# Kernel tuning notes

Hardware: AMD Instinct MI355X
Metric: run time of the kernel (lower is better)

## Reference

```python
import jax, jax.numpy as jnp
import numpy as np

B, N, R = 16, 512, 10
DE, DR, DOUT = 256, 64, 256

def setup_inputs() -> dict:
    key = jax.random.key(0)
    k1, k2, k3, k4 = jax.random.split(key, 4)
    node_features = jax.random.normal(k1, (B, N, DE), dtype=jnp.float32)
    relation_features = jax.random.normal(k2, (B, R, DR), dtype=jnp.float32)
    adj = jax.random.uniform(k3, (B, R, N, N), dtype=jnp.float32)
    in_dim = (DE + DR) * R
    bound = float(np.sqrt(6.0 / (in_dim + DOUT)))  # xavier_uniform
    W = jax.random.uniform(k4, (DOUT, in_dim), dtype=jnp.float32, minval=-bound, maxval=bound)
    bias = jnp.zeros((DOUT,), dtype=jnp.float32)
    return {"node_features": node_features, "relation_features": relation_features,
            "adj": adj, "W": W, "bias": bias}

def reference(node_features, relation_features, adj, W, bias):
    # adj: [B,R,N,N]; node_features: [B,N,De]; relation_features: [B,R,Dr]
    # Per relation r: bmm(adj[:,r], cat([node, rel_r broadcast], -1))
    # Node part: adj @ node_features for every relation at once.
    node_part = jnp.einsum('brnm,bmd->brnd', adj, node_features)      # [B,R,N,De]
    # Relation part: adj @ (rel_r repeated over rows) == rowsum(adj) * rel_r
    rel_part = adj.sum(axis=-1)[..., None] * relation_features[:, :, None, :]  # [B,R,N,Dr]
    supports = jnp.concatenate([node_part, rel_part], axis=-1)        # [B,R,N,De+Dr]
    supports = supports.transpose(0, 2, 1, 3).reshape(node_features.shape[0],
                                                      node_features.shape[1], -1)  # [B,N,R*(De+Dr)]
    return supports @ W.T + bias
```

## Files before the change

kernel.cpp:

```cpp
#include <hip/hip_runtime.h>
#include <stdint.h>

#define B_     16
#define N_     512
#define R_     10
#define DE_    256
#define DR_    64
#define DOUT_  256
#define INDIM_ 3200
#define BLK_   320
#define RN_    5120
#define SPLITS_ 4
#define CPS_    20

typedef __bf16          v8bf  __attribute__((ext_vector_type(8)));
typedef unsigned short  v8us  __attribute__((ext_vector_type(8)));
typedef unsigned short  v4us  __attribute__((ext_vector_type(4)));
typedef float           f32x4 __attribute__((ext_vector_type(4)));

static __device__ __forceinline__ unsigned short f2b(float f) {
  union { float f; unsigned u; } c; c.f = f;
  unsigned r = c.u + 0x7FFFu + ((c.u >> 16) & 1u);
  return (unsigned short)(r >> 16);
}

static __device__ __forceinline__ v8bf us2bf(v8us u) {
  union { v8us u; v8bf b; } c; c.u = u; return c.b;
}

static __device__ __forceinline__ void gl_lds16(const void* g, void* l) {
  __builtin_amdgcn_global_load_lds(
      (const __attribute__((address_space(1))) void*)g,
      (__attribute__((address_space(3))) void*)l, 16, 0, 0);
}

static __device__ __forceinline__ void waitv4() { asm volatile("s_waitcnt vmcnt(4)" ::: "memory"); }
static __device__ __forceinline__ void waitv0() { asm volatile("s_waitcnt vmcnt(0)" ::: "memory"); }
static __device__ __forceinline__ void waitl0() { asm volatile("s_waitcnt lgkmcnt(0)" ::: "memory"); }
#define SCHED0() __builtin_amdgcn_sched_barrier(0)

__global__ void prep_all(const float* __restrict__ nf, const float* __restrict__ W,
                         const float* __restrict__ rel,
                         unsigned short* __restrict__ nodeB,
                         unsigned short* __restrict__ WnB,
                         float* __restrict__ Uf) {
  const int bb = blockIdx.x;
  const int tid = threadIdx.x;
  if (bb < 256) {
    const size_t base = (size_t)bb * 8192;
#pragma unroll
    for (int p = 0; p < 4; ++p) {
      size_t off = base + (size_t)p * 2048 + (size_t)tid * 8;
      float4 x = *(const float4*)(nf + off);
      float4 y = *(const float4*)(nf + off + 4);
      v8us u;
      u[0] = f2b(x.x); u[1] = f2b(x.y); u[2] = f2b(x.z); u[3] = f2b(x.w);
      u[4] = f2b(y.x); u[5] = f2b(y.y); u[6] = f2b(y.z); u[7] = f2b(y.w);
      *(v8us*)(nodeB + off) = u;
    }
  } else if (bb < 896) {
    int idx = (bb - 256) * 1024 + tid * 4;
    int r = idx >> 16;
    int o = (idx >> 8) & 255;
    int d = idx & 255;
    float4 x = *(const float4*)(W + (size_t)o * INDIM_ + r * BLK_ + d);
    v4us u;
    u[0] = f2b(x.x); u[1] = f2b(x.y); u[2] = f2b(x.z); u[3] = f2b(x.w);
    *(v4us*)(WnB + idx) = u;
  } else {
    int idx = (bb - 896) * 256 + tid;
    int o  = idx & 255;
    int br = idx >> 8;
    int r  = br % R_;
    const float* rp = rel + (size_t)br * DR_;
    const float* wp = W + (size_t)o * INDIM_ + r * BLK_ + DE_;
    float v = 0.f;
#pragma unroll 8
    for (int d = 0; d < DR_; ++d) v += rp[d] * wp[d];
    Uf[idx] = v;
  }
}

__global__ void stageA_gemm(const unsigned short* __restrict__ nodeB,
                            const unsigned short* __restrict__ WnB,
                            const float* __restrict__ Uf,
                            unsigned short* __restrict__ Gp) {
  __shared__ unsigned short S[128 * 128];
  unsigned short* Al = S;
  unsigned short* Bl = S + 128 * 64;
  const int br = blockIdx.x;
  const int b  = br / R_, r = br % R_;
  const int o0 = blockIdx.y * 128;
  const int m0 = blockIdx.z * 128;
  const int tid  = threadIdx.x;
  const int lane = tid & 63;
  const int wave = tid >> 6;
  const int wm = wave >> 1, wn = wave & 1;
  const int quad = lane >> 4, l16 = lane & 15;

  const unsigned short* Wb = WnB + (size_t)r * (DOUT_ * DE_);
  const unsigned short* Nb = nodeB + (size_t)b * (N_ * DE_);

  f32x4 acc[4][4];
#pragma unroll
  for (int i = 0; i < 4; ++i)
#pragma unroll
    for (int j = 0; j < 4; ++j) acc[i][j] = f32x4{0.f, 0.f, 0.f, 0.f};

  for (int dk = 0; dk < DE_; dk += 64) {
#pragma unroll
    for (int it = 0; it < 4; ++it) {
      int rowblk = it * 32 + wave * 8;
      int rl = rowblk + (lane >> 3);
      int kc = (lane & 7) ^ (rl & 7);
      gl_lds16(Wb + (size_t)(o0 + rl) * DE_ + dk + kc * 8, Al + rowblk * 64);
      gl_lds16(Nb + (size_t)(m0 + rl) * DE_ + dk + kc * 8, Bl + rowblk * 64);
    }
    __syncthreads();
#pragma unroll
    for (int ks = 0; ks < 2; ++ks) {
      const int kb = ks * 4;
      v8bf av[4], bv[4];
#pragma unroll
      for (int mi = 0; mi < 4; ++mi) {
        int m = wm * 64 + mi * 16 + l16;
        av[mi] = us2bf(*(const v8us*)(Al + m * 64 + (((kb + quad) ^ (m & 7)) * 8)));
      }
#pragma unroll
      for (int ni = 0; ni < 4; ++ni) {
        int c = wn * 64 + ni * 16 + l16;
        bv[ni] = us2bf(*(const v8us*)(Bl + c * 64 + (((kb + quad) ^ (c & 7)) * 8)));
      }
#pragma unroll
      for (int mi = 0; mi < 4; ++mi)
#pragma unroll
        for (int ni = 0; ni < 4; ++ni)
          acc[mi][ni] = __builtin_amdgcn_mfma_f32_16x16x32_bf16(av[mi], bv[ni], acc[mi][ni], 0, 0, 0);
    }
    __syncthreads();
  }

#pragma unroll
  for (int mi = 0; mi < 4; ++mi)
#pragma unroll
    for (int t = 0; t < 4; ++t) {
      int o_loc = wm * 64 + mi * 16 + quad * 4 + t;
      float u = Uf[(size_t)br * DOUT_ + o0 + o_loc];
#pragma unroll
      for (int ni = 0; ni < 4; ++ni) {
        int m_loc = wn * 64 + ni * 16 + l16;
        S[o_loc * 128 + m_loc] = f2b(acc[mi][ni][t] + u);
      }
    }
  __syncthreads();
#pragma unroll
  for (int p = 0; p < 8; ++p) {
    int idx16 = p * 2048 + tid * 8;
    int orow = idx16 >> 7;
    int moff = idx16 & 127;
    unsigned short* dst = Gp + ((size_t)(b * DOUT_ + o0 + orow)) * RN_ + r * N_ + m0 + moff;
    *(v8us*)dst = *(const v8us*)(S + idx16);
  }
}

__global__ __launch_bounds__(512, 1)
void stageB_gemm(const float* __restrict__ adj,
                 const unsigned short* __restrict__ Gp,
                 float* __restrict__ part) {
  __shared__ unsigned short SB[2 * 24576];
  const int b  = blockIdx.x;
  const int n0 = blockIdx.y * 128;
  const int sp = blockIdx.z;
  const int tid  = threadIdx.x;
  const int lane = tid & 63;
  const int wave = tid >> 6;
  const int wm = wave >> 2;
  const int wn = wave & 3;
  const int quad = lane >> 4, l16 = lane & 15;

  const float* Ab = adj + (size_t)b * (R_ * N_ * N_);
  const unsigned short* Gb = Gp + (size_t)b * (DOUT_ * RN_);

  f32x4 acc[4][4];
#pragma unroll
  for (int i = 0; i < 4; ++i)
#pragma unroll
    for (int j = 0; j < 4; ++j) acc[i][j] = f32x4{0.f, 0.f, 0.f, 0.f};

  const int ar0 = tid >> 3;
  const int ac8 = tid & 7;
  const int acs = ac8 ^ (ar0 & 7);
  const int brl = wave * 8 + (lane >> 3);
  const int bkc = lane & 7;
  const int c0 = sp * CPS_;

  float4 As0[4], As1[4];

#define ISSUE_B(slot, cc) do { \
    unsigned short* Bd = SB + (slot) * 24576 + 8192; \
    const int k0b = (cc) << 6; \
    _Pragma("unroll") \
    for (int s = 0; s < 4; ++s) { \
      int rl = s * 64 + brl; \
      int kc = bkc ^ (rl & 7); \
      gl_lds16(Gb + (size_t)rl * RN_ + k0b + kc * 8, Bd + (s * 64 + wave * 8) * 64); \
    } } while (0)

#define ISSUE_A(AR, cc) do { \
    const float* g = Ab + ((size_t)((cc) >> 3) * N_ + n0) * N_ + ((cc) & 7) * 64 \
                     + (size_t)ar0 * N_ + ac8 * 8; \
    AR[0] = *(const float4*)(g); \
    AR[1] = *(const float4*)(g + 4); \
    AR[2] = *(const float4*)(g + 64 * N_); \
    AR[3] = *(const float4*)(g + 64 * N_ + 4); } while (0)

#define CONV_A(AR, slot) do { \
    v8us u0, u1; \
    u0[0] = f2b(AR[0].x); u0[1] = f2b(AR[0].y); u0[2] = f2b(AR[0].z); u0[3] = f2b(AR[0].w); \
    u0[4] = f2b(AR[1].x); u0[5] = f2b(AR[1].y); u0[6] = f2b(AR[1].z); u0[7] = f2b(AR[1].w); \
    u1[0] = f2b(AR[2].x); u1[1] = f2b(AR[2].y); u1[2] = f2b(AR[2].z); u1[3] = f2b(AR[2].w); \
    u1[4] = f2b(AR[3].x); u1[5] = f2b(AR[3].y); u1[6] = f2b(AR[3].z); u1[7] = f2b(AR[3].w); \
    unsigned short* Ad = SB + (slot) * 24576; \
    *(v8us*)(Ad + ar0 * 64 + acs * 8) = u0; \
    *(v8us*)(Ad + (ar0 + 64) * 64 + acs * 8) = u1; } while (0)

#define COMPUTE(slot) do { \
    const unsigned short* Alc = SB + (slot) * 24576; \
    const unsigned short* Blc = Alc + 8192; \
    _Pragma("unroll") \
    for (int ks = 0; ks < 2; ++ks) { \
      const int kb = ks * 4; \
      v8bf av[4], bv[4]; \
      _Pragma("unroll") \
      for (int mi = 0; mi < 4; ++mi) { \
        int m = wm * 64 + mi * 16 + l16; \
        av[mi] = us2bf(*(const v8us*)(Alc + m * 64 + (((kb + quad) ^ (m & 7)) * 8))); \
      } \
      _Pragma("unroll") \
      for (int ni = 0; ni < 4; ++ni) { \
        int o = wn * 64 + ni * 16 + l16; \
        bv[ni] = us2bf(*(const v8us*)(Blc + o * 64 + (((kb + quad) ^ (o & 7)) * 8))); \
      } \
      _Pragma("unroll") \
      for (int mi = 0; mi < 4; ++mi) \
        _Pragma("unroll") \
        for (int ni = 0; ni < 4; ++ni) \
          acc[mi][ni] = __builtin_amdgcn_mfma_f32_16x16x32_bf16(av[mi], bv[ni], acc[mi][ni], 0, 0, 0); \
    } } while (0)

  ISSUE_A(As0, c0 + 0);
  ISSUE_B(0, c0 + 0);
  ISSUE_A(As1, c0 + 1);
  waitv4();
  SCHED0();
  CONV_A(As0, 0);
  waitl0();
  __builtin_amdgcn_s_barrier();

  for (int t = 0; t < CPS_; t += 2) {
    {
      ISSUE_B(1, c0 + t + 1);
      if (t + 2 < CPS_) ISSUE_A(As0, c0 + t + 2);
      SCHED0();
      COMPUTE(0);
      if (t + 2 < CPS_) waitv4();
      else              waitv0();
      SCHED0();
      CONV_A(As1, 1);
      waitl0();
      __builtin_amdgcn_s_barrier();
    }
    {
      if (t + 2 < CPS_) {
        ISSUE_B(0, c0 + t + 2);
        if (t + 3 < CPS_) ISSUE_A(As1, c0 + t + 3);
        SCHED0();
        COMPUTE(1);
        if (t + 3 < CPS_) waitv4();
        else              waitv0();
        SCHED0();
        CONV_A(As0, 0);
        waitl0();
        __builtin_amdgcn_s_barrier();
      } else {
        SCHED0();
        COMPUTE(1);
      }
    }
  }

#undef ISSUE_B
#undef ISSUE_A
#undef CONV_A
#undef COMPUTE

  float* pb = part + (((size_t)sp * B_ + b) * N_) * DOUT_;
#pragma unroll
  for (int mi = 0; mi < 4; ++mi)
#pragma unroll
    for (int t4 = 0; t4 < 4; ++t4) {
      int row = n0 + wm * 64 + mi * 16 + quad * 4 + t4;
#pragma unroll
      for (int ni = 0; ni < 4; ++ni) {
        int col = wn * 64 + ni * 16 + l16;
        pb[(size_t)row * DOUT_ + col] = acc[mi][ni][t4];
      }
    }
}

__global__ void reduce_out(const float* __restrict__ part, const float* __restrict__ bias,
                           float* __restrict__ out) {
  const size_t idx = (size_t)blockIdx.x * 256 + threadIdx.x;
  const size_t stride = (size_t)B_ * N_ * DOUT_ / 4;
  f32x4 a = *(const f32x4*)(bias + (idx & 63) * 4);
#pragma unroll
  for (int s = 0; s < SPLITS_; ++s) {
    f32x4 p = *(const f32x4*)((const float*)part + (stride * s + idx) * 4);
    a += p;
  }
  *(f32x4*)(out + idx * 4) = a;
}

extern "C" void kernel_launch(void* const* d_in, const int* in_sizes, int n_in,
                              void* d_out, int out_size, void* d_ws, size_t ws_size,
                              hipStream_t stream) {
  const float* node = (const float*)d_in[0];
  const float* rel  = (const float*)d_in[1];
  const float* adj  = (const float*)d_in[2];
  const float* W    = (const float*)d_in[3];
  const float* bias = (const float*)d_in[4];
  float* out = (float*)d_out;

  char* ws = (char*)d_ws;
  unsigned short* nodeB = (unsigned short*)(ws);
  unsigned short* WnB   = (unsigned short*)(ws + ((size_t)5 << 20));
  float*          Uf    = (float*)         (ws + ((size_t)7 << 20));
  unsigned short* Gp    = (unsigned short*)(ws + ((size_t)8 << 20));
  float*          part  = (float*)         (ws + ((size_t)48 << 20));

  prep_all<<<dim3(1056), 256, 0, stream>>>(node, W, rel, nodeB, WnB, Uf);
  stageA_gemm<<<dim3(B_ * R_, DOUT_ / 128, N_ / 128), 256, 0, stream>>>(nodeB, WnB, Uf, Gp);
  stageB_gemm<<<dim3(B_, N_ / 128, SPLITS_), 512, 0, stream>>>(adj, Gp, part);
  reduce_out<<<dim3((B_ * N_ * DOUT_ / 4) / 256), 256, 0, stream>>>(part, bias, out);
}
```

Before: 291.2 us.

## Reuse node tile across five relations in stage A with double-buffered W loads

Stage A now has each block keep a full 64-row node tile (all 256 K) resident in LDS and loop over five relations. It streams the per-relation W slices through a double buffer, prefetching the next K-chunk while MFMAs run on the current one. This cuts repeated global loads of node features and overlaps W loads with compute. The trade-offs are a smaller N tile per wave, fewer blocks in the grid (512 instead of 1280), and more LDS per block.

Result: no change. 289.5 us (-0.6%).

```diff
diff --git a/kernel.cpp b/kernel.cpp
--- a/kernel.cpp
+++ b/kernel.cpp
@@ -85,81 +85,116 @@
                             const unsigned short* __restrict__ WnB,
                             const float* __restrict__ Uf,
                             unsigned short* __restrict__ Gp) {
-  __shared__ unsigned short S[128 * 128];
-  unsigned short* Al = S;
-  unsigned short* Bl = S + 128 * 64;
-  const int br = blockIdx.x;
-  const int b  = br / R_, r = br % R_;
+  __shared__ unsigned short S[40960];
+  unsigned short* NodeP = S;
+  unsigned short* Wbuf  = S + 16384;
+  unsigned short* Cb    = S + 32768;
+  const int b  = blockIdx.x;
   const int o0 = blockIdx.y * 128;
-  const int m0 = blockIdx.z * 128;
+  const int m0 = (blockIdx.z & 7) * 64;
+  const int r0 = (blockIdx.z >> 3) * 5;
   const int tid  = threadIdx.x;
   const int lane = tid & 63;
   const int wave = tid >> 6;
   const int wm = wave >> 1, wn = wave & 1;
   const int quad = lane >> 4, l16 = lane & 15;
-
-  const unsigned short* Wb = WnB + (size_t)r * (DOUT_ * DE_);
+  const int srl = lane >> 3;
+  const int skc = lane & 7;
+
   const unsigned short* Nb = nodeB + (size_t)b * (N_ * DE_);
 
-  f32x4 acc[4][4];
-#pragma unroll
-  for (int i = 0; i < 4; ++i)
-#pragma unroll
-    for (int j = 0; j < 4; ++j) acc[i][j] = f32x4{0.f, 0.f, 0.f, 0.f};
-
-  for (int dk = 0; dk < DE_; dk += 64) {
+#pragma unroll
+  for (int p = 0; p < 4; ++p)
+#pragma unroll
+    for (int it = 0; it < 2; ++it) {
+      int rowblk = it * 32 + wave * 8;
+      int rl = rowblk + srl;
+      int kc = skc ^ (rl & 7);
+      gl_lds16(Nb + (size_t)(m0 + rl) * DE_ + p * 64 + kc * 8,
+               NodeP + p * 4096 + rowblk * 64);
+    }
+  {
+    const unsigned short* Wb = WnB + (size_t)r0 * (DOUT_ * DE_);
 #pragma unroll
     for (int it = 0; it < 4; ++it) {
       int rowblk = it * 32 + wave * 8;
-      int rl = rowblk + (lane >> 3);
-      int kc = (lane & 7) ^ (rl & 7);
-      gl_lds16(Wb + (size_t)(o0 + rl) * DE_ + dk + kc * 8, Al + rowblk * 64);
-      gl_lds16(Nb + (size_t)(m0 + rl) * DE_ + dk + kc * 8, Bl + rowblk * 64);
-    }
+      int rl = rowblk + srl;
+      int kc = skc ^ (rl & 7);
+      gl_lds16(Wb + (size_t)(o0 + rl) * DE_ + kc * 8, Wbuf + rowblk * 64);
+    }
+  }
+  __syncthreads();
+
+  for (int rr = 0; rr < 5; ++rr) {
+    const int r = r0 + rr;
+    f32x4 acc[4][2];
+#pragma unroll
+    for (int i = 0; i < 4; ++i)
+#pragma unroll
+      for (int j = 0; j < 2; ++j) acc[i][j] = f32x4{0.f, 0.f, 0.f, 0.f};
+
+#pragma unroll
+    for (int t = 0; t < 4; ++t) {
+      if (rr < 4 || t < 3) {
+        const int nr = (t < 3) ? r : (r + 1);
+        const int nt = (t < 3) ? (t + 1) : 0;
+        const unsigned short* Wb = WnB + (size_t)nr * (DOUT_ * DE_);
+        unsigned short* Wd = Wbuf + ((t + 1) & 1) * 8192;
+#pragma unroll
+        for (int it = 0; it < 4; ++it) {
+          int rowblk = it * 32 + wave * 8;
+          int rl = rowblk + srl;
+          int kc = skc ^ (rl & 7);
+          gl_lds16(Wb + (size_t)(o0 + rl) * DE_ + nt * 64 + kc * 8, Wd + rowblk * 64);
+        }
+      }
+      const unsigned short* Wc = Wbuf + (t & 1) * 8192;
+      const unsigned short* Np = NodeP + t * 4096;
+#pragma unroll
+      for (int ks = 0; ks < 2; ++ks) {
+        const int kb = ks * 4;
+        v8bf av[4], bv[2];
+#pragma unroll
+        for (int mi = 0; mi < 4; ++mi) {
+          int m = wm * 64 + mi * 16 + l16;
+          av[mi] = us2bf(*(const v8us*)(Wc + m * 64 + (((kb + quad) ^ (m & 7)) * 8)));
+        }
+#pragma unroll
+        for (int ni = 0; ni < 2; ++ni) {
+          int c = wn * 32 + ni * 16 + l16;
+          bv[ni] = us2bf(*(const v8us*)(Np + c * 64 + (((kb + quad) ^ (c & 7)) * 8)));
+        }
+#pragma unroll
+        for (int mi = 0; mi < 4; ++mi)
+#pragma unroll
+          for (int ni = 0; ni < 2; ++ni)
+            acc[mi][ni] = __builtin_amdgcn_mfma_f32_16x16x32_bf16(av[mi], bv[ni], acc[mi][ni], 0, 0, 0);
+      }
+      __syncthreads();
+    }
+
+#pragma unroll
+    for (int mi = 0; mi < 4; ++mi)
+#pragma unroll
+      for (int tt = 0; tt < 4; ++tt) {
+        int o_loc = wm * 64 + mi * 16 + quad * 4 + tt;
+        float u = Uf[((size_t)b * R_ + r) * DOUT_ + o0 + o_loc];
+#pragma unroll
+        for (int ni = 0; ni < 2; ++ni) {
+          int m_loc = wn * 32 + ni * 16 + l16;
+          Cb[o_loc * 64 + m_loc] = f2b(acc[mi][ni][tt] + u);
+        }
+      }
     __syncthreads();
 #pragma unroll
-    for (int ks = 0; ks < 2; ++ks) {
-      const int kb = ks * 4;
-      v8bf av[4], bv[4];
-#pragma unroll
-      for (int mi = 0; mi < 4; ++mi) {
-        int m = wm * 64 + mi * 16 + l16;
-        av[mi] = us2bf(*(const v8us*)(Al + m * 64 + (((kb + quad) ^ (m & 7)) * 8)));
-      }
-#pragma unroll
-      for (int ni = 0; ni < 4; ++ni) {
-        int c = wn * 64 + ni * 16 + l16;
-        bv[ni] = us2bf(*(const v8us*)(Bl + c * 64 + (((kb + quad) ^ (c & 7)) * 8)));
-      }
-#pragma unroll
-      for (int mi = 0; mi < 4; ++mi)
-#pragma unroll
-        for (int ni = 0; ni < 4; ++ni)
-          acc[mi][ni] = __builtin_amdgcn_mfma_f32_16x16x32_bf16(av[mi], bv[ni], acc[mi][ni], 0, 0, 0);
+    for (int p = 0; p < 4; ++p) {
+      int idx16 = p * 2048 + tid * 8;
+      int orow = idx16 >> 6;
+      int moff = idx16 & 63;
+      unsigned short* dst = Gp + ((size_t)(b * DOUT_ + o0 + orow)) * RN_ + r * N_ + m0 + moff;
+      *(v8us*)dst = *(const v8us*)(Cb + idx16);
     }
     __syncthreads();
-  }
-
-#pragma unroll
-  for (int mi = 0; mi < 4; ++mi)
-#pragma unroll
-    for (int t = 0; t < 4; ++t) {
-      int o_loc = wm * 64 + mi * 16 + quad * 4 + t;
-      float u = Uf[(size_t)br * DOUT_ + o0 + o_loc];
-#pragma unroll
-      for (int ni = 0; ni < 4; ++ni) {
-        int m_loc = wn * 64 + ni * 16 + l16;
-        S[o_loc * 128 + m_loc] = f2b(acc[mi][ni][t] + u);
-      }
-    }
-  __syncthreads();
-#pragma unroll
-  for (int p = 0; p < 8; ++p) {
-    int idx16 = p * 2048 + tid * 8;
-    int orow = idx16 >> 7;
-    int moff = idx16 & 127;
-    unsigned short* dst = Gp + ((size_t)(b * DOUT_ + o0 + orow)) * RN_ + r * N_ + m0 + moff;
-    *(v8us*)dst = *(const v8us*)(S + idx16);
   }
 }
 
@@ -339,7 +374,7 @@
   float*          part  = (float*)         (ws + ((size_t)48 << 20));
 
   prep_all<<<dim3(1056), 256, 0, stream>>>(node, W, rel, nodeB, WnB, Uf);
-  stageA_gemm<<<dim3(B_ * R_, DOUT_ / 128, N_ / 128), 256, 0, stream>>>(nodeB, WnB, Uf, Gp);
+  stageA_gemm<<<dim3(B_, 2, 16), 256, 0, stream>>>(nodeB, WnB, Uf, Gp);
   stageB_gemm<<<dim3(B_, N_ / 128, SPLITS_), 512, 0, stream>>>(adj, Gp, part);
   reduce_out<<<dim3((B_ * N_ * DOUT_ / 4) / 256), 256, 0, stream>>>(part, bias, out);
 }
```
